# Kernel tuning notes

Hardware: AMD Instinct MI355X
Metric: run time of the kernel (lower is better)

Reference implementation:

```python
import jax, jax.numpy as jnp
import numpy as np

DIM = 512
NUM_EXPERTS = 16
HIDDEN = 512
OUT_DIM = DIM // 4  # 128


def setup_inputs() -> dict:
    key = jax.random.key(0)
    k_x, k_w1, k_w2 = jax.random.split(key, 3)
    x = jax.random.normal(k_x, (4, 2048, DIM), dtype=jnp.float32)
    # init_(t): uniform(-1/sqrt(last_dim), 1/sqrt(last_dim))
    s1 = 1.0 / np.sqrt(HIDDEN)
    s2 = 1.0 / np.sqrt(OUT_DIM)
    w1 = jax.random.uniform(k_w1, (NUM_EXPERTS, DIM, HIDDEN), dtype=jnp.float32, minval=-s1, maxval=s1)
    w2 = jax.random.uniform(k_w2, (NUM_EXPERTS, HIDDEN, OUT_DIM), dtype=jnp.float32, minval=-s2, maxval=s2)
    return {"x": x, "w1": w1, "w2": w2}


def reference(x, w1, w2):
    # x: [b, n, d]; w1: [e, d, h]; w2: [e, h, d4]
    hidden = jnp.einsum("bnd,edh->benh", x, w1)          # [b, e, n, h]
    hidden = jax.nn.gelu(hidden, approximate=False)       # exact GELU = torch nn.GELU default
    out = jnp.einsum("benh,ehd->bnde", hidden, w2)        # [b, n, d4, e]
    return out
```

## Files before the change

kernel.cpp:

```cpp
#include <hip/hip_runtime.h>
#include <stdint.h>

typedef short bf16x8 __attribute__((ext_vector_type(8)));
typedef float f32x4 __attribute__((ext_vector_type(4)));

__device__ __forceinline__ void async_cp16(const void* g, short* lds) {
  __builtin_amdgcn_global_load_lds(
      (const __attribute__((address_space(1))) void*)g,
      (__attribute__((address_space(3))) void*)lds, 16, 0, 0);
}

__device__ __forceinline__ float gelu_f(float v) {
  float z = 1.5957691216057308f * (v + 0.044715f * v * v * v);
  return __fdividef(v, 1.0f + __expf(-z));
}

__device__ __forceinline__ short f2bf(float x) {
  uint32_t u = __float_as_uint(x);
  u += 0x7fffu + ((u >> 16) & 1u);
  return (short)(u >> 16);
}

__global__ __launch_bounds__(256)
void prep_all(const float* __restrict__ x, const float* __restrict__ w1,
              const float* __restrict__ w2, short* __restrict__ Xb,
              short* __restrict__ w1t, short* __restrict__ w2t)
{
  __shared__ __align__(16) short T[64][72];
  const int b = blockIdx.x;
  const int t = threadIdx.x;

  if (b < 2048) {
    const int idx = (b * 256 + t) * 8;
    bf16x8 o;
#pragma unroll
    for (int u = 0; u < 8; ++u) o[u] = f2bf(x[idx + u]);
    *(bf16x8*)(Xb + idx) = o;
    return;
  }

  const float* src; short* dst; int e, r0, c0, R, C;
  if (b < 3072) {
    int idx = b - 2048; e = idx >> 6; int rem = idx & 63;
    r0 = (rem >> 3) * 64; c0 = (rem & 7) * 64; R = 512; C = 512;
    src = w1; dst = w1t;
  } else {
    int idx = b - 3072; e = idx >> 4; int rem = idx & 15;
    r0 = (rem >> 1) * 64; c0 = (rem & 1) * 64; R = 512; C = 128;
    src = w2; dst = w2t;
  }
  const float* s = src + (size_t)e * R * C;
  short* d       = dst + (size_t)e * R * C;
  const int i = t >> 3, j8 = t & 7;
#pragma unroll
  for (int p = 0; p < 2; ++p) {
    int ii = i + p * 32;
#pragma unroll
    for (int u = 0; u < 8; ++u)
      T[ii][j8 * 8 + u] = f2bf(s[(size_t)(r0 + ii) * C + c0 + j8 * 8 + u]);
  }
  __syncthreads();
#pragma unroll
  for (int p = 0; p < 2; ++p) {
    int ii = i + p * 32;
    bf16x8 v;
#pragma unroll
    for (int u = 0; u < 8; ++u) v[u] = T[j8 * 8 + u][ii];
    *(bf16x8*)(d + (size_t)(c0 + ii) * R + r0 + j8 * 8) = v;
  }
}

__global__ __launch_bounds__(256, 2)
void moe_kernel(const short* __restrict__ Xb, const short* __restrict__ W1T,
                const short* __restrict__ W2T, void* __restrict__ O, int staged)
{
  __shared__ __align__(16) short SM[25600];
  short* const Ws0 = SM;
  short* const Ws1 = SM + 4096;
  short* const Xs0 = SM + 8192;
  short* const Xs1 = SM + 12288;
  short* const HL  = SM + 8192;

  const int tid = threadIdx.x;
  const int l = tid & 63, w = tid >> 6;
  const int wm = w & 1, wn = w >> 1;
  const int e    = blockIdx.x >> 6;
  const int tile = blockIdx.x & 63;

  const int lrow = l >> 2, lq = l & 3;
  int ldso[2];
  const char *xg[2], *w1g[2], *w2g[2];
#pragma unroll
  for (int c = 0; c < 2; ++c) {
    int prow = w * 32 + c * 16 + lrow;
    int qg = lq ^ ((prow >> 1) & 3);
    ldso[c] = (w * 32 + c * 16) * 32;
    xg[c]  = (const char*)Xb  + (size_t)(tile * 128 + prow) * 1024 + qg * 16;
    w1g[c] = (const char*)W1T + (size_t)e * 524288 + (size_t)prow * 1024 + qg * 16;
    w2g[c] = (const char*)W2T + (size_t)e * 131072 + (size_t)prow * 1024 + qg * 16;
  }

  const int lm = l & 15;
  const int slot = (l >> 4) ^ ((lm >> 1) & 3);
  const int aoff = (wm * 64 + lm) * 32 + slot * 8;
  const int boff = (wn * 64 + lm) * 32 + slot * 8;
  const int hro  = (wm * 64 + lm) * 136 + (l >> 4) * 8;
  const int hwo  = (wm * 64 + (l >> 4) * 4) * 136 + wn * 64 + lm;

  f32x4 acc2[4][4];
#pragma unroll
  for (int i = 0; i < 4; ++i)
#pragma unroll
    for (int j = 0; j < 4; ++j) acc2[i][j] = (f32x4){0.f, 0.f, 0.f, 0.f};

#pragma unroll
  for (int c = 0; c < 2; ++c) {
    async_cp16(xg[c],  Xs0 + ldso[c]);
    async_cp16(w1g[c], Ws0 + ldso[c]);
  }

  for (int hc = 0; hc < 4; ++hc) {
    f32x4 acc1[4][4];
#pragma unroll
    for (int i = 0; i < 4; ++i)
#pragma unroll
      for (int j = 0; j < 4; ++j) acc1[i][j] = (f32x4){0.f, 0.f, 0.f, 0.f};

    const size_t w1hc = (size_t)hc * 131072;

#pragma unroll
    for (int kk = 0; kk < 16; ++kk) {
      __syncthreads();
      if (kk < 15) {
        short* xb = ((kk + 1) & 1) ? Xs1 : Xs0;
        short* wb = ((kk + 1) & 1) ? Ws1 : Ws0;
#pragma unroll
        for (int c = 0; c < 2; ++c) {
          async_cp16(xg[c] + (kk + 1) * 64,         xb + ldso[c]);
          async_cp16(w1g[c] + w1hc + (kk + 1) * 64, wb + ldso[c]);
        }
      } else {
#pragma unroll
        for (int c = 0; c < 2; ++c)
          async_cp16(w2g[c] + hc * 256, Ws0 + ldso[c]);
      }
      const short* xb = (kk & 1) ? Xs1 : Xs0;
      const short* wb = (kk & 1) ? Ws1 : Ws0;
      bf16x8 af[4], bfr[4];
#pragma unroll
      for (int t = 0; t < 4; ++t) af[t]  = *(const bf16x8*)(xb + aoff + t * 512);
#pragma unroll
      for (int t = 0; t < 4; ++t) bfr[t] = *(const bf16x8*)(wb + boff + t * 512);
#pragma unroll
      for (int i = 0; i < 4; ++i)
#pragma unroll
        for (int j = 0; j < 4; ++j)
          acc1[i][j] = __builtin_amdgcn_mfma_f32_16x16x32_bf16(af[i], bfr[j], acc1[i][j], 0, 0, 0);
    }

    __syncthreads();

#pragma unroll
    for (int i = 0; i < 4; ++i)
#pragma unroll
      for (int j = 0; j < 4; ++j)
#pragma unroll
        for (int r = 0; r < 4; ++r)
          HL[hwo + i * 2176 + r * 136 + j * 16] = f2bf(gelu_f(acc1[i][j][r]));

#pragma unroll
    for (int s = 0; s < 4; ++s) {
      __syncthreads();
      if (s < 3) {
        short* wb = ((s + 1) & 1) ? Ws1 : Ws0;
#pragma unroll
        for (int c = 0; c < 2; ++c)
          async_cp16(w2g[c] + hc * 256 + (s + 1) * 64, wb + ldso[c]);
      }
      const short* wb = (s & 1) ? Ws1 : Ws0;
      bf16x8 af[4], bfr[4];
#pragma unroll
      for (int t = 0; t < 4; ++t) af[t]  = *(const bf16x8*)(HL + hro + t * 2176 + s * 32);
#pragma unroll
      for (int t = 0; t < 4; ++t) bfr[t] = *(const bf16x8*)(wb + boff + t * 512);
#pragma unroll
      for (int i = 0; i < 4; ++i)
#pragma unroll
        for (int j = 0; j < 4; ++j)
          acc2[i][j] = __builtin_amdgcn_mfma_f32_16x16x32_bf16(af[i], bfr[j], acc2[i][j], 0, 0, 0);
    }

    if (hc < 3) {
      __syncthreads();
#pragma unroll
      for (int c = 0; c < 2; ++c) {
        async_cp16(xg[c],                              Xs0 + ldso[c]);
        async_cp16(w1g[c] + (size_t)(hc + 1) * 131072, Ws0 + ldso[c]);
      }
    }
  }

  const int d4 = wn * 64 + lm;
  const int lqr = (l >> 4) * 4;
  if (staged) {
    unsigned short* Ob = (unsigned short*)O;
    const size_t base = ((size_t)e * 8192 + tile * 128 + wm * 64 + lqr) * 128 + d4;
#pragma unroll
    for (int i = 0; i < 4; ++i)
#pragma unroll
      for (int r = 0; r < 4; ++r)
#pragma unroll
        for (int j = 0; j < 4; ++j)
          Ob[base + (size_t)(i * 16 + r) * 128 + j * 16] = (unsigned short)f2bf(acc2[i][j][r]);
  } else {
    float* Of = (float*)O;
    const size_t rowb = (size_t)tile * 128 + wm * 64 + lqr;
    const size_t base = (rowb * 128 + d4) * 16 + e;
#pragma unroll
    for (int i = 0; i < 4; ++i)
#pragma unroll
      for (int r = 0; r < 4; ++r)
#pragma unroll
        for (int j = 0; j < 4; ++j)
          Of[base + (size_t)(i * 16 + r) * 2048 + j * 256] = acc2[i][j][r];
  }
}

__global__ __launch_bounds__(256, 2)
void permute_kernel(const unsigned short* __restrict__ OUTs, float* __restrict__ OUT)
{
  __shared__ float T[8 * 16 * 132];
  const int t = threadIdx.x;
  const int r0 = blockIdx.x * 8;
#pragma unroll
  for (int it = 0; it < 8; ++it) {
    int v = it * 256 + t;
    int e = v >> 7, rem = v & 127, r = rem >> 4, q8 = rem & 15;
    bf16x8 d = *(const bf16x8*)(OUTs + ((size_t)e * 8192 + r0 + r) * 128 + q8 * 8);
#pragma unroll
    for (int u = 0; u < 8; ++u)
      T[(r * 16 + e) * 132 + q8 * 8 + u] =
          __uint_as_float(((uint32_t)(unsigned short)d[u]) << 16);
  }
  __syncthreads();
#pragma unroll
  for (int it = 0; it < 16; ++it) {
    int u = it * 256 + t;
    int r = u >> 9;
    int c4 = (u & 511) * 4;
    int d4 = c4 >> 4, e0 = c4 & 15;
    f32x4 o;
#pragma unroll
    for (int i = 0; i < 4; ++i) o[i] = T[(r * 16 + e0 + i) * 132 + d4];
    *(f32x4*)(OUT + (size_t)(r0 + r) * 2048 + c4) = o;
  }
}

extern "C" void kernel_launch(void* const* d_in, const int* in_sizes, int n_in,
                              void* d_out, int out_size, void* d_ws, size_t ws_size,
                              hipStream_t stream)
{
  const float* x  = (const float*)d_in[0];
  const float* w1 = (const float*)d_in[1];
  const float* w2 = (const float*)d_in[2];
  float* out = (float*)d_out;

  short* Xb  = (short*)d_ws;
  short* w1t = Xb + 4194304;
  short* w2t = w1t + 4194304;
  unsigned short* OUTs = (unsigned short*)((char*)d_ws + 18874368);
  const bool staged = ws_size >= 52428800ULL;

  prep_all<<<dim3(3328), 256, 0, stream>>>(x, w1, w2, Xb, w1t, w2t);
  moe_kernel<<<dim3(1024), 256, 0, stream>>>(Xb, w1t, w2t,
                                             staged ? (void*)OUTs : (void*)out,
                                             staged ? 1 : 0);
  if (staged)
    permute_kernel<<<dim3(1024), 256, 0, stream>>>(OUTs, out);
}
```

Measured before the change: 226.3 us.

## Triple-buffer LDS tiles with prefetch distance two and explicit vmcnt barriers

Replaces the double-buffered X/W1/W2 staging with three LDS buffers and issues async global-to-LDS copies two steps ahead, including prefetching the W2 chunks and the next hidden-chunk's first tiles during the second GEMM. The __syncthreads calls become partial s_waitcnt vmcnt waits plus raw barriers, so loads can stay in flight across iterations. The GELU staging area is remapped so the barrier before it can be dropped. The cost is more LDS per block, which could limit occupancy, and the last iteration prefetches W1 data past the current expert, which may read beyond the buffer for the final expert.

```diff
diff --git a/kernel.cpp b/kernel.cpp
--- a/kernel.cpp
+++ b/kernel.cpp
@@ -20,6 +20,13 @@
   u += 0x7fffu + ((u >> 16) & 1u);
   return (short)(u >> 16);
 }
+
+#define WAIT_BAR_V4() do { asm volatile("s_waitcnt vmcnt(4) lgkmcnt(0)" ::: "memory"); \
+  __builtin_amdgcn_s_barrier(); asm volatile("" ::: "memory"); } while (0)
+#define WAIT_BAR_V2() do { asm volatile("s_waitcnt vmcnt(2) lgkmcnt(0)" ::: "memory"); \
+  __builtin_amdgcn_s_barrier(); asm volatile("" ::: "memory"); } while (0)
+#define BAR_L0() do { asm volatile("s_waitcnt lgkmcnt(0)" ::: "memory"); \
+  __builtin_amdgcn_s_barrier(); asm volatile("" ::: "memory"); } while (0)
 
 __global__ __launch_bounds__(256)
 void prep_all(const float* __restrict__ x, const float* __restrict__ w1,
@@ -74,12 +81,14 @@
 void moe_kernel(const short* __restrict__ Xb, const short* __restrict__ W1T,
                 const short* __restrict__ W2T, void* __restrict__ O, int staged)
 {
-  __shared__ __align__(16) short SM[25600];
+  __shared__ __align__(16) short SM[33792];
   short* const Ws0 = SM;
   short* const Ws1 = SM + 4096;
-  short* const Xs0 = SM + 8192;
-  short* const Xs1 = SM + 12288;
-  short* const HL  = SM + 8192;
+  short* const Ws2 = SM + 8192;
+  short* const Xs0 = SM + 12288;
+  short* const Xs1 = SM + 16384;
+  short* const Xs2 = SM + 20480;
+  short* const HL  = SM + 16384;
 
   const int tid = threadIdx.x;
   const int l = tid & 63, w = tid >> 6;
@@ -115,8 +124,13 @@
 
 #pragma unroll
   for (int c = 0; c < 2; ++c) {
-    async_cp16(xg[c],  Xs0 + ldso[c]);
-    async_cp16(w1g[c], Ws0 + ldso[c]);
+    async_cp16(xg[c],       Xs0 + ldso[c]);
+    async_cp16(w1g[c],      Ws0 + ldso[c]);
+  }
+#pragma unroll
+  for (int c = 0; c < 2; ++c) {
+    async_cp16(xg[c] + 64,  Xs1 + ldso[c]);
+    async_cp16(w1g[c] + 64, Ws1 + ldso[c]);
   }
 
   for (int hc = 0; hc < 4; ++hc) {
@@ -130,22 +144,26 @@
 
 #pragma unroll
     for (int kk = 0; kk < 16; ++kk) {
-      __syncthreads();
-      if (kk < 15) {
-        short* xb = ((kk + 1) & 1) ? Xs1 : Xs0;
-        short* wb = ((kk + 1) & 1) ? Ws1 : Ws0;
+      if (kk == 15) { WAIT_BAR_V2(); } else { WAIT_BAR_V4(); }
+      if (kk < 14) {
+        short* xb = ((kk + 2) % 3 == 0) ? Xs0 : ((kk + 2) % 3 == 1) ? Xs1 : Xs2;
+        short* wb = ((kk + 2) % 3 == 0) ? Ws0 : ((kk + 2) % 3 == 1) ? Ws1 : Ws2;
 #pragma unroll
         for (int c = 0; c < 2; ++c) {
-          async_cp16(xg[c] + (kk + 1) * 64,         xb + ldso[c]);
-          async_cp16(w1g[c] + w1hc + (kk + 1) * 64, wb + ldso[c]);
+          async_cp16(xg[c] + (kk + 2) * 64,         xb + ldso[c]);
+          async_cp16(w1g[c] + w1hc + (kk + 2) * 64, wb + ldso[c]);
         }
+      } else if (kk == 14) {
+#pragma unroll
+        for (int c = 0; c < 2; ++c)
+          async_cp16(w2g[c] + hc * 256,      Ws1 + ldso[c]);
       } else {
 #pragma unroll
         for (int c = 0; c < 2; ++c)
-          async_cp16(w2g[c] + hc * 256, Ws0 + ldso[c]);
+          async_cp16(w2g[c] + hc * 256 + 64, Ws2 + ldso[c]);
       }
-      const short* xb = (kk & 1) ? Xs1 : Xs0;
-      const short* wb = (kk & 1) ? Ws1 : Ws0;
+      const short* xb = (kk % 3 == 0) ? Xs0 : (kk % 3 == 1) ? Xs1 : Xs2;
+      const short* wb = (kk % 3 == 0) ? Ws0 : (kk % 3 == 1) ? Ws1 : Ws2;
       bf16x8 af[4], bfr[4];
 #pragma unroll
       for (int t = 0; t < 4; ++t) af[t]  = *(const bf16x8*)(xb + aoff + t * 512);
@@ -158,8 +176,6 @@
           acc1[i][j] = __builtin_amdgcn_mfma_f32_16x16x32_bf16(af[i], bfr[j], acc1[i][j], 0, 0, 0);
     }
 
-    __syncthreads();
-
 #pragma unroll
     for (int i = 0; i < 4; ++i)
 #pragma unroll
@@ -170,14 +186,25 @@
 
 #pragma unroll
     for (int s = 0; s < 4; ++s) {
-      __syncthreads();
-      if (s < 3) {
-        short* wb = ((s + 1) & 1) ? Ws1 : Ws0;
-#pragma unroll
-        for (int c = 0; c < 2; ++c)
-          async_cp16(w2g[c] + hc * 256 + (s + 1) * 64, wb + ldso[c]);
+      WAIT_BAR_V2();
+      if (s == 0) {
+#pragma unroll
+        for (int c = 0; c < 2; ++c)
+          async_cp16(w2g[c] + hc * 256 + 128, Ws0 + ldso[c]);
+      } else if (s == 1) {
+#pragma unroll
+        for (int c = 0; c < 2; ++c)
+          async_cp16(w2g[c] + hc * 256 + 192, Ws1 + ldso[c]);
+      } else if (s == 2) {
+#pragma unroll
+        for (int c = 0; c < 2; ++c)
+          async_cp16(xg[c], Xs0 + ldso[c]);
+      } else {
+#pragma unroll
+        for (int c = 0; c < 2; ++c)
+          async_cp16(w1g[c] + w1hc + 131072, Ws0 + ldso[c]);
       }
-      const short* wb = (s & 1) ? Ws1 : Ws0;
+      const short* wb = (s == 0) ? Ws1 : (s == 1) ? Ws2 : (s == 2) ? Ws0 : Ws1;
       bf16x8 af[4], bfr[4];
 #pragma unroll
       for (int t = 0; t < 4; ++t) af[t]  = *(const bf16x8*)(HL + hro + t * 2176 + s * 32);
@@ -190,15 +217,15 @@
           acc2[i][j] = __builtin_amdgcn_mfma_f32_16x16x32_bf16(af[i], bfr[j], acc2[i][j], 0, 0, 0);
     }
 
-    if (hc < 3) {
-      __syncthreads();
-#pragma unroll
-      for (int c = 0; c < 2; ++c) {
-        async_cp16(xg[c],                              Xs0 + ldso[c]);
-        async_cp16(w1g[c] + (size_t)(hc + 1) * 131072, Ws0 + ldso[c]);
-      }
+    BAR_L0();
+#pragma unroll
+    for (int c = 0; c < 2; ++c) {
+      async_cp16(xg[c] + 64,                  Xs1 + ldso[c]);
+      async_cp16(w1g[c] + w1hc + 131072 + 64, Ws1 + ldso[c]);
     }
   }
+
+  asm volatile("s_waitcnt vmcnt(0)" ::: "memory");
 
   const int d4 = wn * 64 + lm;
   const int lqr = (l >> 4) * 4;
```

New measurement: 245.6 us. +8.6%, slower.

## Double K-step per LDS stage and switch to XOR-swizzled layout for hidden buffer

Applied to the files above, without the earlier changes.

Raises the K chunk per pipeline stage from 32 to 64 elements, which halves the number of barrier-separated steps in both GEMM phases. It also replaces the padded hidden-activation buffer with an XOR-swizzled layout to avoid bank conflicts. The second GEMM now uses two stages, with its second W2 slice prefetched while GELU runs. LDS per block grows from 50KB to 64KB, which at two blocks per CU approaches the LDS capacity.

```diff
diff --git a/kernel.cpp b/kernel.cpp
--- a/kernel.cpp
+++ b/kernel.cpp
@@ -74,12 +74,12 @@
 void moe_kernel(const short* __restrict__ Xb, const short* __restrict__ W1T,
                 const short* __restrict__ W2T, void* __restrict__ O, int staged)
 {
-  __shared__ __align__(16) short SM[25600];
+  __shared__ __align__(16) short SM[32768];
   short* const Ws0 = SM;
-  short* const Ws1 = SM + 4096;
-  short* const Xs0 = SM + 8192;
-  short* const Xs1 = SM + 12288;
-  short* const HL  = SM + 8192;
+  short* const Ws1 = SM + 8192;
+  short* const Xs0 = SM + 16384;
+  short* const Xs1 = SM + 24576;
+  char*  const HLb = (char*)(SM + 16384);
 
   const int tid = threadIdx.x;
   const int l = tid & 63, w = tid >> 6;
@@ -87,25 +87,28 @@
   const int e    = blockIdx.x >> 6;
   const int tile = blockIdx.x & 63;
 
-  const int lrow = l >> 2, lq = l & 3;
-  int ldso[2];
-  const char *xg[2], *w1g[2], *w2g[2];
-#pragma unroll
-  for (int c = 0; c < 2; ++c) {
-    int prow = w * 32 + c * 16 + lrow;
-    int qg = lq ^ ((prow >> 1) & 3);
-    ldso[c] = (w * 32 + c * 16) * 32;
-    xg[c]  = (const char*)Xb  + (size_t)(tile * 128 + prow) * 1024 + qg * 16;
-    w1g[c] = (const char*)W1T + (size_t)e * 524288 + (size_t)prow * 1024 + qg * 16;
-    w2g[c] = (const char*)W2T + (size_t)e * 131072 + (size_t)prow * 1024 + qg * 16;
-  }
-
-  const int lm = l & 15;
-  const int slot = (l >> 4) ^ ((lm >> 1) & 3);
-  const int aoff = (wm * 64 + lm) * 32 + slot * 8;
-  const int boff = (wn * 64 + lm) * 32 + slot * 8;
-  const int hro  = (wm * 64 + lm) * 136 + (l >> 4) * 8;
-  const int hwo  = (wm * 64 + (l >> 4) * 4) * 136 + wn * 64 + lm;
+  const int lr8 = l >> 3, gs = (l & 7) ^ lr8;
+  int ldso[4];
+  const char *xg[4], *w1g[4], *w2g[4];
+#pragma unroll
+  for (int c = 0; c < 4; ++c) {
+    int p = c * 4 + w;
+    int row = p * 8 + lr8;
+    ldso[c] = p * 512;
+    xg[c]  = (const char*)Xb  + (size_t)(tile * 128 + row) * 1024 + gs * 16;
+    w1g[c] = (const char*)W1T + (size_t)e * 524288 + (size_t)row * 1024 + gs * 16;
+    w2g[c] = (const char*)W2T + (size_t)e * 131072 + (size_t)row * 1024 + gs * 16;
+  }
+
+  const int lm = l & 15, g = l >> 4;
+  int sA[2], sB[2];
+#pragma unroll
+  for (int ks = 0; ks < 2; ++ks) {
+    int sl = (ks * 4 + g) ^ (lm & 7);
+    sA[ks] = (wm * 64 + lm) * 64 + sl * 8;
+    sB[ks] = (wn * 64 + lm) * 64 + sl * 8;
+  }
+  const int hswz = (lm & 7) << 4;
 
   f32x4 acc2[4][4];
 #pragma unroll
@@ -114,10 +117,9 @@
     for (int j = 0; j < 4; ++j) acc2[i][j] = (f32x4){0.f, 0.f, 0.f, 0.f};
 
 #pragma unroll
-  for (int c = 0; c < 2; ++c) {
-    async_cp16(xg[c],  Xs0 + ldso[c]);
-    async_cp16(w1g[c], Ws0 + ldso[c]);
-  }
+  for (int c = 0; c < 4; ++c) async_cp16(xg[c],  Xs0 + ldso[c]);
+#pragma unroll
+  for (int c = 0; c < 4; ++c) async_cp16(w1g[c], Ws0 + ldso[c]);
 
   for (int hc = 0; hc < 4; ++hc) {
     f32x4 acc1[4][4];
@@ -126,82 +128,95 @@
 #pragma unroll
       for (int j = 0; j < 4; ++j) acc1[i][j] = (f32x4){0.f, 0.f, 0.f, 0.f};
 
-    const size_t w1hc = (size_t)hc * 131072;
-
-#pragma unroll
-    for (int kk = 0; kk < 16; ++kk) {
+    const size_t w1o = (size_t)hc * 131072;
+
+#pragma unroll
+    for (int kk = 0; kk < 8; ++kk) {
       __syncthreads();
-      if (kk < 15) {
+      if (kk < 7) {
         short* xb = ((kk + 1) & 1) ? Xs1 : Xs0;
         short* wb = ((kk + 1) & 1) ? Ws1 : Ws0;
 #pragma unroll
-        for (int c = 0; c < 2; ++c) {
-          async_cp16(xg[c] + (kk + 1) * 64,         xb + ldso[c]);
-          async_cp16(w1g[c] + w1hc + (kk + 1) * 64, wb + ldso[c]);
-        }
+        for (int c = 0; c < 4; ++c)
+          async_cp16(xg[c] + (kk + 1) * 128,        xb + ldso[c]);
+#pragma unroll
+        for (int c = 0; c < 4; ++c)
+          async_cp16(w1g[c] + w1o + (kk + 1) * 128, wb + ldso[c]);
       } else {
 #pragma unroll
-        for (int c = 0; c < 2; ++c)
+        for (int c = 0; c < 4; ++c)
           async_cp16(w2g[c] + hc * 256, Ws0 + ldso[c]);
       }
       const short* xb = (kk & 1) ? Xs1 : Xs0;
       const short* wb = (kk & 1) ? Ws1 : Ws0;
-      bf16x8 af[4], bfr[4];
-#pragma unroll
-      for (int t = 0; t < 4; ++t) af[t]  = *(const bf16x8*)(xb + aoff + t * 512);
-#pragma unroll
-      for (int t = 0; t < 4; ++t) bfr[t] = *(const bf16x8*)(wb + boff + t * 512);
-#pragma unroll
-      for (int i = 0; i < 4; ++i)
-#pragma unroll
-        for (int j = 0; j < 4; ++j)
-          acc1[i][j] = __builtin_amdgcn_mfma_f32_16x16x32_bf16(af[i], bfr[j], acc1[i][j], 0, 0, 0);
-    }
-
-    __syncthreads();
-
-#pragma unroll
-    for (int i = 0; i < 4; ++i)
-#pragma unroll
-      for (int j = 0; j < 4; ++j)
-#pragma unroll
-        for (int r = 0; r < 4; ++r)
-          HL[hwo + i * 2176 + r * 136 + j * 16] = f2bf(gelu_f(acc1[i][j][r]));
-
-#pragma unroll
-    for (int s = 0; s < 4; ++s) {
-      __syncthreads();
-      if (s < 3) {
-        short* wb = ((s + 1) & 1) ? Ws1 : Ws0;
-#pragma unroll
-        for (int c = 0; c < 2; ++c)
-          async_cp16(w2g[c] + hc * 256 + (s + 1) * 64, wb + ldso[c]);
-      }
-      const short* wb = (s & 1) ? Ws1 : Ws0;
-      bf16x8 af[4], bfr[4];
-#pragma unroll
-      for (int t = 0; t < 4; ++t) af[t]  = *(const bf16x8*)(HL + hro + t * 2176 + s * 32);
-#pragma unroll
-      for (int t = 0; t < 4; ++t) bfr[t] = *(const bf16x8*)(wb + boff + t * 512);
-#pragma unroll
-      for (int i = 0; i < 4; ++i)
-#pragma unroll
-        for (int j = 0; j < 4; ++j)
-          acc2[i][j] = __builtin_amdgcn_mfma_f32_16x16x32_bf16(af[i], bfr[j], acc2[i][j], 0, 0, 0);
-    }
-
-    if (hc < 3) {
-      __syncthreads();
-#pragma unroll
-      for (int c = 0; c < 2; ++c) {
-        async_cp16(xg[c],                              Xs0 + ldso[c]);
-        async_cp16(w1g[c] + (size_t)(hc + 1) * 131072, Ws0 + ldso[c]);
+#pragma unroll
+      for (int ks = 0; ks < 2; ++ks) {
+        bf16x8 af[4], bfr[4];
+#pragma unroll
+        for (int t = 0; t < 4; ++t) af[t]  = *(const bf16x8*)(xb + sA[ks] + t * 1024);
+#pragma unroll
+        for (int t = 0; t < 4; ++t) bfr[t] = *(const bf16x8*)(wb + sB[ks] + t * 1024);
+#pragma unroll
+        for (int i = 0; i < 4; ++i)
+#pragma unroll
+          for (int j = 0; j < 4; ++j)
+            acc1[i][j] = __builtin_amdgcn_mfma_f32_16x16x32_bf16(af[i], bfr[j], acc1[i][j], 0, 0, 0);
       }
     }
+
+    __syncthreads();
+
+#pragma unroll
+    for (int c = 0; c < 4; ++c)
+      async_cp16(w2g[c] + hc * 256 + 128, Ws1 + ldso[c]);
+
+#pragma unroll
+    for (int i = 0; i < 4; ++i)
+#pragma unroll
+      for (int j = 0; j < 4; ++j)
+#pragma unroll
+        for (int r = 0; r < 4; ++r) {
+          int tok = wm * 64 + i * 16 + g * 4 + r;
+          int h   = wn * 64 + j * 16 + lm;
+          int byo = (tok * 256 + h * 2) ^ ((tok & 7) << 4);
+          *(short*)(HLb + byo) = f2bf(gelu_f(acc1[i][j][r]));
+        }
+
+    __syncthreads();
+
+#pragma unroll
+    for (int s = 0; s < 2; ++s) {
+      const short* wb = s ? Ws1 : Ws0;
+#pragma unroll
+      for (int ks = 0; ks < 2; ++ks) {
+        bf16x8 af[4], bfr[4];
+#pragma unroll
+        for (int t = 0; t < 4; ++t) {
+          int tok = wm * 64 + t * 16 + lm;
+          int byo = (tok * 256 + s * 128 + ks * 64 + g * 16) ^ hswz;
+          af[t] = *(const bf16x8*)(HLb + byo);
+        }
+#pragma unroll
+        for (int t = 0; t < 4; ++t) bfr[t] = *(const bf16x8*)(wb + sB[ks] + t * 1024);
+#pragma unroll
+        for (int i = 0; i < 4; ++i)
+#pragma unroll
+          for (int j = 0; j < 4; ++j)
+            acc2[i][j] = __builtin_amdgcn_mfma_f32_16x16x32_bf16(af[i], bfr[j], acc2[i][j], 0, 0, 0);
+      }
+    }
+
+    __syncthreads();
+    if (hc < 3) {
+#pragma unroll
+      for (int c = 0; c < 4; ++c) async_cp16(xg[c], Xs0 + ldso[c]);
+#pragma unroll
+      for (int c = 0; c < 4; ++c) async_cp16(w1g[c] + w1o + 131072, Ws0 + ldso[c]);
+    }
   }
 
   const int d4 = wn * 64 + lm;
-  const int lqr = (l >> 4) * 4;
+  const int lqr = g * 4;
   if (staged) {
     unsigned short* Ob = (unsigned short*)O;
     const size_t base = ((size_t)e * 8192 + tile * 128 + wm * 64 + lqr) * 128 + d4;
```

Result: slower. 341.5 us (+50.9%).

## Load W2 fragments directly to registers and overlap next X/W1 prefetch with GEMM2

Applied to the files above, without the earlier changes.

The W2 operand for the second GEMM is now read straight from global memory into registers instead of staged through double-buffered LDS. The hidden tile gets its own LDS region, so the next chunk's X/W1 prefetch can start right after the GELU write and overlap the second GEMM. This removes four barriers per hidden chunk. MFMA sections are wrapped in s_setprio to favour the matrix issue. In exchange, LDS use grows (which may cut occupancy), register pressure rises from the 16 held W2 fragments, and global W2 reads are no longer coalesced through LDS.

```diff
diff --git a/kernel.cpp b/kernel.cpp
--- a/kernel.cpp
+++ b/kernel.cpp
@@ -74,12 +74,12 @@
 void moe_kernel(const short* __restrict__ Xb, const short* __restrict__ W1T,
                 const short* __restrict__ W2T, void* __restrict__ O, int staged)
 {
-  __shared__ __align__(16) short SM[25600];
+  __shared__ __align__(16) short SM[33792];
   short* const Ws0 = SM;
   short* const Ws1 = SM + 4096;
   short* const Xs0 = SM + 8192;
   short* const Xs1 = SM + 12288;
-  short* const HL  = SM + 8192;
+  short* const HL  = SM + 16384;
 
   const int tid = threadIdx.x;
   const int l = tid & 63, w = tid >> 6;
@@ -89,7 +89,7 @@
 
   const int lrow = l >> 2, lq = l & 3;
   int ldso[2];
-  const char *xg[2], *w1g[2], *w2g[2];
+  const char *xg[2], *w1g[2];
 #pragma unroll
   for (int c = 0; c < 2; ++c) {
     int prow = w * 32 + c * 16 + lrow;
@@ -97,7 +97,6 @@
     ldso[c] = (w * 32 + c * 16) * 32;
     xg[c]  = (const char*)Xb  + (size_t)(tile * 128 + prow) * 1024 + qg * 16;
     w1g[c] = (const char*)W1T + (size_t)e * 524288 + (size_t)prow * 1024 + qg * 16;
-    w2g[c] = (const char*)W2T + (size_t)e * 131072 + (size_t)prow * 1024 + qg * 16;
   }
 
   const int lm = l & 15;
@@ -107,6 +106,9 @@
   const int hro  = (wm * 64 + lm) * 136 + (l >> 4) * 8;
   const int hwo  = (wm * 64 + (l >> 4) * 4) * 136 + wn * 64 + lm;
 
+  const char* w2r_base = (const char*)W2T + (size_t)e * 131072 +
+                         (size_t)(wn * 64 + lm) * 1024 + (l >> 4) * 16;
+
   f32x4 acc2[4][4];
 #pragma unroll
   for (int i = 0; i < 4; ++i)
@@ -139,10 +141,6 @@
           async_cp16(xg[c] + (kk + 1) * 64,         xb + ldso[c]);
           async_cp16(w1g[c] + w1hc + (kk + 1) * 64, wb + ldso[c]);
         }
-      } else {
-#pragma unroll
-        for (int c = 0; c < 2; ++c)
-          async_cp16(w2g[c] + hc * 256, Ws0 + ldso[c]);
       }
       const short* xb = (kk & 1) ? Xs1 : Xs0;
       const short* wb = (kk & 1) ? Ws1 : Ws0;
@@ -151,14 +149,21 @@
       for (int t = 0; t < 4; ++t) af[t]  = *(const bf16x8*)(xb + aoff + t * 512);
 #pragma unroll
       for (int t = 0; t < 4; ++t) bfr[t] = *(const bf16x8*)(wb + boff + t * 512);
+      __builtin_amdgcn_s_setprio(1);
 #pragma unroll
       for (int i = 0; i < 4; ++i)
 #pragma unroll
         for (int j = 0; j < 4; ++j)
           acc1[i][j] = __builtin_amdgcn_mfma_f32_16x16x32_bf16(af[i], bfr[j], acc1[i][j], 0, 0, 0);
+      __builtin_amdgcn_s_setprio(0);
     }
 
-    __syncthreads();
+    bf16x8 w2r[4][4];
+#pragma unroll
+    for (int s = 0; s < 2; ++s)
+#pragma unroll
+      for (int t = 0; t < 4; ++t)
+        w2r[s][t] = *(const bf16x8*)(w2r_base + (size_t)t * 16384 + hc * 256 + s * 64);
 
 #pragma unroll
     for (int i = 0; i < 4; ++i)
@@ -168,35 +173,34 @@
         for (int r = 0; r < 4; ++r)
           HL[hwo + i * 2176 + r * 136 + j * 16] = f2bf(gelu_f(acc1[i][j][r]));
 
-#pragma unroll
-    for (int s = 0; s < 4; ++s) {
-      __syncthreads();
-      if (s < 3) {
-        short* wb = ((s + 1) & 1) ? Ws1 : Ws0;
-#pragma unroll
-        for (int c = 0; c < 2; ++c)
-          async_cp16(w2g[c] + hc * 256 + (s + 1) * 64, wb + ldso[c]);
-      }
-      const short* wb = (s & 1) ? Ws1 : Ws0;
-      bf16x8 af[4], bfr[4];
-#pragma unroll
-      for (int t = 0; t < 4; ++t) af[t]  = *(const bf16x8*)(HL + hro + t * 2176 + s * 32);
-#pragma unroll
-      for (int t = 0; t < 4; ++t) bfr[t] = *(const bf16x8*)(wb + boff + t * 512);
-#pragma unroll
-      for (int i = 0; i < 4; ++i)
-#pragma unroll
-        for (int j = 0; j < 4; ++j)
-          acc2[i][j] = __builtin_amdgcn_mfma_f32_16x16x32_bf16(af[i], bfr[j], acc2[i][j], 0, 0, 0);
-    }
+    __syncthreads();
 
     if (hc < 3) {
-      __syncthreads();
 #pragma unroll
       for (int c = 0; c < 2; ++c) {
         async_cp16(xg[c],                              Xs0 + ldso[c]);
         async_cp16(w1g[c] + (size_t)(hc + 1) * 131072, Ws0 + ldso[c]);
       }
+    }
+
+#pragma unroll
+    for (int s = 2; s < 4; ++s)
+#pragma unroll
+      for (int t = 0; t < 4; ++t)
+        w2r[s][t] = *(const bf16x8*)(w2r_base + (size_t)t * 16384 + hc * 256 + s * 64);
+
+#pragma unroll
+    for (int s = 0; s < 4; ++s) {
+      bf16x8 af[4];
+#pragma unroll
+      for (int t = 0; t < 4; ++t) af[t] = *(const bf16x8*)(HL + hro + t * 2176 + s * 32);
+      __builtin_amdgcn_s_setprio(1);
+#pragma unroll
+      for (int i = 0; i < 4; ++i)
+#pragma unroll
+        for (int j = 0; j < 4; ++j)
+          acc2[i][j] = __builtin_amdgcn_mfma_f32_16x16x32_bf16(af[i], w2r[s][j], acc2[i][j], 0, 0, 0);
+      __builtin_amdgcn_s_setprio(0);
     }
   }
 
```

Result: slower. 235.1 us (+3.9%).
